# Kernel tuning notes

Hardware: AMD Instinct MI355X
Metric: run time of the kernel (lower is better)

The kernel has to match this reference:

```python
import jax, jax.numpy as jnp
import numpy as np
from jax.scipy.special import logsumexp

NUM_TAGS = 64
BATCH = 512
SEQ = 1024


def setup_inputs() -> dict:
    key = jax.random.key(0)
    k1, k2, k3, k4, k5 = jax.random.split(key, 5)
    emissions = jax.random.normal(k1, (BATCH, SEQ, NUM_TAGS), dtype=jnp.float32)
    # parameters: uniform(-0.1, 0.1) as in reset_parameters
    start_transitions = jax.random.uniform(k2, (NUM_TAGS,), minval=-0.1, maxval=0.1, dtype=jnp.float32)
    end_transitions = jax.random.uniform(k3, (NUM_TAGS,), minval=-0.1, maxval=0.1, dtype=jnp.float32)
    transitions = jax.random.uniform(k4, (NUM_TAGS, NUM_TAGS), minval=-0.1, maxval=0.1, dtype=jnp.float32)
    tags = jax.random.randint(k5, (BATCH, SEQ), 0, NUM_TAGS, dtype=jnp.int64)
    mask = jnp.ones((BATCH, SEQ), dtype=bool)
    return {"emissions": emissions, "start_transitions": start_transitions,
            "end_transitions": end_transitions, "transitions": transitions,
            "tags": tags, "mask": mask}


def _crf_loss(emissions, start_transitions, end_transitions, transitions, tags, mask):
    # batch_first=True -> move to time-major (S, B, T)
    emissions = jnp.transpose(emissions, (1, 0, 2))
    tags = tags.T
    mask = mask.T
    S, B, T = emissions.shape
    maskf = mask.astype(emissions.dtype)

    # ---- joint (numerator) score, fully vectorized ----
    em_sc = jnp.take_along_axis(emissions, tags[:, :, None], axis=2)[:, :, 0]  # [S, B]
    trans_sc = transitions[tags[:-1], tags[1:]]                                # [S-1, B]
    score = start_transitions[tags[0]] + em_sc[0]
    score = score + ((trans_sc + em_sc[1:]) * maskf[1:]).sum(axis=0)
    seq_ends = mask.astype(jnp.int32).sum(axis=0) - 1                          # [B]
    last_tags = tags[seq_ends, jnp.arange(B)]
    score = score + end_transitions[last_tags]

    # ---- log partition (denominator) via scan over time ----
    def step(alphas, xs):
        em_i, m_i = xs  # em_i: [B, T], m_i: [B]
        inner = alphas[:, :, None] + transitions[None, :, :] + em_i[:, None, :]  # [B, T, T]
        new_alphas = logsumexp(inner, axis=1)
        return jnp.where(m_i[:, None], new_alphas, alphas), None

    alphas0 = start_transitions + emissions[0]  # [B, T]
    alphas, _ = jax.lax.scan(step, alphas0, (emissions[1:], mask[1:]))
    log_z = logsumexp(alphas + end_transitions, axis=1)  # [B]

    return (log_z - score).sum()  # reduction='sum'


def reference(emissions, start_transitions, end_transitions, transitions, tags, mask):
    return _crf_loss(emissions, start_transitions, end_transitions, transitions, tags, mask)
```

## Files before the change

kernel.cpp:

```cpp
#include <hip/hip_runtime.h>

#define NT 64
#define SEQ 1024
#define BATCH 512

typedef _Float16 h2 __attribute__((ext_vector_type(2)));
typedef _Float16 h8 __attribute__((ext_vector_type(8)));

__device__ __forceinline__ float rlf(float v, int lane) {
  return __int_as_float(__builtin_amdgcn_readlane(__float_as_int(v), lane));
}
__device__ __forceinline__ float bsum(float v) {
  #pragma unroll
  for (int m = 32; m; m >>= 1) v += __shfl_xor(v, m);
  return v;
}
__device__ __forceinline__ float dot2(h2 a, h2 b, float c) {
#if __has_builtin(__builtin_amdgcn_fdot2)
  return __builtin_amdgcn_fdot2(a, b, c, false);
#else
  return fmaf((float)a[0], (float)b[0], fmaf((float)a[1], (float)b[1], c));
#endif
}

__global__ __launch_bounds__(64) void crf_fwd(
    const float* __restrict__ em,
    const float* __restrict__ startT,
    const float* __restrict__ endT,
    const float* __restrict__ trans,
    const int*   __restrict__ tags,
    float* __restrict__ ws)
{
  const int b = blockIdx.x;
  const int j = threadIdx.x;

  __shared__ float sT[NT * NT];
  __shared__ alignas(16) _Float16 sH[NT];
  for (int i = j; i < NT * NT; i += NT) sT[i] = trans[i];
  __syncthreads();

  h2 eth[NT / 2];
  #pragma unroll
  for (int p = 0; p < NT / 2; ++p) {
    eth[p][0] = (_Float16)(__expf(sT[(2 * p + 0) * NT + j]) * 0.015625f);
    eth[p][1] = (_Float16)(__expf(sT[(2 * p + 1) * NT + j]) * 0.015625f);
  }

  const float* emb = em + (size_t)b * SEQ * NT;
  const int*   tgb = tags + (size_t)b * SEQ;

  const float stv = startT[j];
  const float alpha0 = stv + emb[j];
  const float c0 = rlf(alpha0, 0);
  float nb = __expf(alpha0 - c0);
  sH[j] = (_Float16)nb;

  float Crn = 0.0f;
  float rr = 1.0f;
  float lgrr = 0.0f;

  int tagv = tgb[j];
  const int tag0 = __builtin_amdgcn_readlane(tagv, 0);
  const float sc0 = rlf(stv, tag0);

  float scp = 0.0f;
  {
    int ptag = __shfl_up(tagv, 1);
    if (j > 0) scp += sT[ptag * NT + tagv];
    scp += emb[j * NT + tagv];
  }
  int carry = __builtin_amdgcn_readlane(tagv, 63);

  float embuf[8];
  #pragma unroll
  for (int k = 1; k <= 8; ++k) embuf[k & 7] = emb[k * NT + j];

  auto step = [&](int s, int slot) {
    const float em_cur = embuf[slot];
    int spre = s + 8;
    if (spre > SEQ - 1) spre = SEQ - 1;
    embuf[slot] = emb[spre * NT + j];

    const float mm = __expf(em_cur - 0.5f) * rr;
    Crn -= lgrr;

    float a[8];
    #pragma unroll
    for (int q = 0; q < 8; ++q) {
      const h8 wv = *reinterpret_cast<const h8*>(&sH[8 * q]);
      const h2 w0 = __builtin_shufflevector(wv, wv, 0, 1);
      const h2 w1 = __builtin_shufflevector(wv, wv, 2, 3);
      const h2 w2 = __builtin_shufflevector(wv, wv, 4, 5);
      const h2 w3 = __builtin_shufflevector(wv, wv, 6, 7);
      float acc = dot2(w0, eth[4 * q + 0], 0.0f);
      acc = dot2(w1, eth[4 * q + 1], acc);
      acc = dot2(w2, eth[4 * q + 2], acc);
      acc = dot2(w3, eth[4 * q + 3], acc);
      a[q] = acc;
    }
    const float s01 = (a[0] + a[1]) + (a[2] + a[3]);
    const float s23 = (a[4] + a[5]) + (a[6] + a[7]);
    nb = (s01 + s23) * mm;
    sH[j] = (_Float16)nb;

    const float rv = rlf(nb, 0);
    rr = __builtin_amdgcn_rcpf(rv);
    lgrr = __logf(rr);
  };

  #pragma unroll 8
  for (int r = 1; r < NT; ++r) step(r, r & 7);

  for (int tb = 1; tb < SEQ / NT; ++tb) {
    tagv = tgb[tb * NT + j];
    int ptag = __shfl_up(tagv, 1);
    if (j == 0) ptag = carry;
    scp += sT[ptag * NT + tagv];
    const int base = tb * NT;
    scp += emb[(base + j) * NT + tagv];
    carry = __builtin_amdgcn_readlane(tagv, 63);

    #pragma unroll 8
    for (int r = 0; r < NT; ++r) step(base + r, r & 7);
  }

  const float endv = endT[j];
  const float x = nb * __expf(endv);
  const float tot = bsum(x);
  const float Cbase = c0 + (float)(SEQ - 1) * (0.5f + 4.1588830833596715f);
  const float logz = Cbase + Crn + __logf(tot);

  const float sctot = bsum(scp);
  const float score = sc0 + sctot + rlf(endv, carry);

  if (j == 0) ws[b] = logz - score;
}

__global__ __launch_bounds__(64) void reduce_loss(const float* __restrict__ ws,
                                                  float* __restrict__ out) {
  const int t = threadIdx.x;
  float v = 0.f;
  #pragma unroll
  for (int k = 0; k < BATCH / 64; ++k) v += ws[k * 64 + t];
  const float tot = bsum(v);
  if (t == 0) out[0] = tot;
}

extern "C" void kernel_launch(void* const* d_in, const int* in_sizes, int n_in,
                              void* d_out, int out_size, void* d_ws, size_t ws_size,
                              hipStream_t stream) {
  const float* em    = (const float*)d_in[0];
  const float* st    = (const float*)d_in[1];
  const float* en    = (const float*)d_in[2];
  const float* tr    = (const float*)d_in[3];
  const int*   tags  = (const int*)d_in[4];

  float* ws  = (float*)d_ws;
  float* out = (float*)d_out;

  crf_fwd<<<BATCH, 64, 0, stream>>>(em, st, en, tr, tags, ws);
  reduce_loss<<<1, 64, 0, stream>>>(ws, out);
}
```

Measured before the change: 363.8 us.

## Replace LDS broadcast matvec with cross-lane butterfly reduction and max renormalization

Drops the shared-memory alpha vector and computes the per-step 64x64 transition matvec in registers. Each lane dot-multiplies its own pair of alphas against an XOR-permuted exp-transition table, then a DPP/ds_swizzle/bpermute butterfly tree reduces the partial sums across lanes. Normalization now uses a wave-wide max in place of lane 0's value, which is more robust numerically but adds a serial chain of six cross-lane ops per step. This removes the LDS write and read and their latency on the recurrence's critical path, in exchange for about 31 extra cross-lane permutes per step.

```diff
diff --git a/kernel.cpp b/kernel.cpp
--- a/kernel.cpp
+++ b/kernel.cpp
@@ -5,7 +5,6 @@
 #define BATCH 512
 
 typedef _Float16 h2 __attribute__((ext_vector_type(2)));
-typedef _Float16 h8 __attribute__((ext_vector_type(8)));
 
 __device__ __forceinline__ float rlf(float v, int lane) {
   return __int_as_float(__builtin_amdgcn_readlane(__float_as_int(v), lane));
@@ -14,6 +13,23 @@
   #pragma unroll
   for (int m = 32; m; m >>= 1) v += __shfl_xor(v, m);
   return v;
+}
+__device__ __forceinline__ float bmax(float v) {
+  #pragma unroll
+  for (int m = 32; m; m >>= 1) v = fmaxf(v, __shfl_xor(v, m));
+  return v;
+}
+template <int IMM>
+__device__ __forceinline__ float swzf(float x) {
+  return __int_as_float(__builtin_amdgcn_ds_swizzle(__float_as_int(x), IMM));
+}
+template <int CTRL>
+__device__ __forceinline__ float dppf(float x) {
+  return __int_as_float(
+      __builtin_amdgcn_update_dpp(0, __float_as_int(x), CTRL, 0xF, 0xF, true));
+}
+__device__ __forceinline__ float bpf(int addr, float x) {
+  return __int_as_float(__builtin_amdgcn_ds_bpermute(addr, __float_as_int(x)));
 }
 __device__ __forceinline__ float dot2(h2 a, h2 b, float c) {
 #if __has_builtin(__builtin_amdgcn_fdot2)
@@ -35,15 +51,17 @@
   const int j = threadIdx.x;
 
   __shared__ float sT[NT * NT];
-  __shared__ alignas(16) _Float16 sH[NT];
   for (int i = j; i < NT * NT; i += NT) sT[i] = trans[i];
   __syncthreads();
 
-  h2 eth[NT / 2];
+  const int bp32 = ((j ^ 32) << 2);
+
+  h2 etx[32];
   #pragma unroll
-  for (int p = 0; p < NT / 2; ++p) {
-    eth[p][0] = (_Float16)(__expf(sT[(2 * p + 0) * NT + j]) * 0.015625f);
-    eth[p][1] = (_Float16)(__expf(sT[(2 * p + 1) * NT + j]) * 0.015625f);
+  for (int r = 0; r < 32; ++r) {
+    const int col = j ^ (2 * r);
+    etx[r][0] = (_Float16)(__expf(sT[j * NT + col]) * 0.015625f);
+    etx[r][1] = (_Float16)(__expf(sT[(j ^ 1) * NT + col]) * 0.015625f);
   }
 
   const float* emb = em + (size_t)b * SEQ * NT;
@@ -51,9 +69,8 @@
 
   const float stv = startT[j];
   const float alpha0 = stv + emb[j];
-  const float c0 = rlf(alpha0, 0);
+  const float c0 = bmax(alpha0);
   float nb = __expf(alpha0 - c0);
-  sH[j] = (_Float16)nb;
 
   float Crn = 0.0f;
   float rr = 1.0f;
@@ -84,27 +101,33 @@
     const float mm = __expf(em_cur - 0.5f) * rr;
     Crn -= lgrr;
 
-    float a[8];
+    const float nbx = dppf<0xB1>(nb);
+    const h2 w2 = __builtin_bit_cast(h2, __builtin_amdgcn_cvt_pkrtz(nb, nbx));
+
+    float A[32];
     #pragma unroll
-    for (int q = 0; q < 8; ++q) {
-      const h8 wv = *reinterpret_cast<const h8*>(&sH[8 * q]);
-      const h2 w0 = __builtin_shufflevector(wv, wv, 0, 1);
-      const h2 w1 = __builtin_shufflevector(wv, wv, 2, 3);
-      const h2 w2 = __builtin_shufflevector(wv, wv, 4, 5);
-      const h2 w3 = __builtin_shufflevector(wv, wv, 6, 7);
-      float acc = dot2(w0, eth[4 * q + 0], 0.0f);
-      acc = dot2(w1, eth[4 * q + 1], acc);
-      acc = dot2(w2, eth[4 * q + 2], acc);
-      acc = dot2(w3, eth[4 * q + 3], acc);
-      a[q] = acc;
-    }
-    const float s01 = (a[0] + a[1]) + (a[2] + a[3]);
-    const float s23 = (a[4] + a[5]) + (a[6] + a[7]);
-    nb = (s01 + s23) * mm;
-    sH[j] = (_Float16)nb;
+    for (int r = 0; r < 32; ++r) A[r] = dot2(w2, etx[r], 0.0f);
 
-    const float rv = rlf(nb, 0);
-    rr = __builtin_amdgcn_rcpf(rv);
+    #pragma unroll
+    for (int r = 0; r < 32; r += 2)  A[r] += dppf<0x4E>(A[r | 1]);
+    #pragma unroll
+    for (int r = 0; r < 32; r += 4)  A[r] += swzf<0x101F>(A[r | 2]);
+    #pragma unroll
+    for (int r = 0; r < 32; r += 8)  A[r] += swzf<0x201F>(A[r | 4]);
+    #pragma unroll
+    for (int r = 0; r < 32; r += 16) A[r] += swzf<0x401F>(A[r | 8]);
+    A[0] += bpf(bp32, A[16]);
+
+    nb = A[0] * mm;
+
+    float mx = nb;
+    mx = fmaxf(mx, swzf<0x041F>(mx));
+    mx = fmaxf(mx, swzf<0x081F>(mx));
+    mx = fmaxf(mx, swzf<0x101F>(mx));
+    mx = fmaxf(mx, swzf<0x201F>(mx));
+    mx = fmaxf(mx, swzf<0x401F>(mx));
+    mx = fmaxf(mx, bpf(bp32, mx));
+    rr = __builtin_amdgcn_rcpf(mx);
     lgrr = __logf(rr);
   };
 
@@ -125,8 +148,7 @@
   }
 
   const float endv = endT[j];
-  const float x = nb * __expf(endv);
-  const float tot = bsum(x);
+  const float tot = bsum(nb * __expf(endv));
   const float Cbase = c0 + (float)(SEQ - 1) * (0.5f + 4.1588830833596715f);
   const float logz = Cbase + Crn + __logf(tot);
 
```

New measurement: 703.7 us. 93.4% more time.

## Replace LDS broadcast of alphas with DPP/bpermute cross-lane matvec

Applied to the files above, without the earlier changes.

Each step no longer writes the scaled alpha vector to shared memory and reads it back as 8 packed loads per lane. Each lane now packs its own value with neighbours obtained through DPP swizzles and computes 16 partial dot products against a transition table whose register layout is permuted by an XOR pattern. The partials are routed to their owning lanes with 15 ds_bpermute operations, summed in a tree, and the unroll factor is reduced to 4. The aim is to shorten the per-step serial dependency through LDS, at the cost of more cross-lane permute traffic per step.

```diff
diff --git a/kernel.cpp b/kernel.cpp
--- a/kernel.cpp
+++ b/kernel.cpp
@@ -5,7 +5,6 @@
 #define BATCH 512
 
 typedef _Float16 h2 __attribute__((ext_vector_type(2)));
-typedef _Float16 h8 __attribute__((ext_vector_type(8)));
 
 __device__ __forceinline__ float rlf(float v, int lane) {
   return __int_as_float(__builtin_amdgcn_readlane(__float_as_int(v), lane));
@@ -15,6 +14,13 @@
   for (int m = 32; m; m >>= 1) v += __shfl_xor(v, m);
   return v;
 }
+template <int CTRL>
+__device__ __forceinline__ int dppi(int x) {
+  return __builtin_amdgcn_update_dpp(0, x, CTRL, 0xF, 0xF, true);
+}
+__device__ __forceinline__ float bpf(int addr, float x) {
+  return __int_as_float(__builtin_amdgcn_ds_bpermute(addr, __float_as_int(x)));
+}
 __device__ __forceinline__ float dot2(h2 a, h2 b, float c) {
 #if __has_builtin(__builtin_amdgcn_fdot2)
   return __builtin_amdgcn_fdot2(a, b, c, false);
@@ -23,7 +29,7 @@
 #endif
 }
 
-__global__ __launch_bounds__(64) void crf_fwd(
+__global__ __launch_bounds__(64, 1) void crf_fwd(
     const float* __restrict__ em,
     const float* __restrict__ startT,
     const float* __restrict__ endT,
@@ -35,16 +41,22 @@
   const int j = threadIdx.x;
 
   __shared__ float sT[NT * NT];
-  __shared__ alignas(16) _Float16 sH[NT];
   for (int i = j; i < NT * NT; i += NT) sT[i] = trans[i];
   __syncthreads();
 
-  h2 eth[NT / 2];
+  h2 etxa[16], etxb[16];
   #pragma unroll
-  for (int p = 0; p < NT / 2; ++p) {
-    eth[p][0] = (_Float16)(__expf(sT[(2 * p + 0) * NT + j]) * 0.015625f);
-    eth[p][1] = (_Float16)(__expf(sT[(2 * p + 1) * NT + j]) * 0.015625f);
+  for (int q = 0; q < 16; ++q) {
+    const int c = j ^ (4 * q);
+    etxa[q][0] = (_Float16)(__expf(sT[(j ^ 0) * NT + c]) * 0.015625f);
+    etxa[q][1] = (_Float16)(__expf(sT[(j ^ 1) * NT + c]) * 0.015625f);
+    etxb[q][0] = (_Float16)(__expf(sT[(j ^ 2) * NT + c]) * 0.015625f);
+    etxb[q][1] = (_Float16)(__expf(sT[(j ^ 3) * NT + c]) * 0.015625f);
   }
+
+  int bpa[16];
+  #pragma unroll
+  for (int q = 0; q < 16; ++q) bpa[q] = (j ^ (4 * q)) << 2;
 
   const float* emb = em + (size_t)b * SEQ * NT;
   const int*   tgb = tags + (size_t)b * SEQ;
@@ -53,7 +65,6 @@
   const float alpha0 = stv + emb[j];
   const float c0 = rlf(alpha0, 0);
   float nb = __expf(alpha0 - c0);
-  sH[j] = (_Float16)nb;
 
   float Crn = 0.0f;
   float rr = 1.0f;
@@ -84,31 +95,33 @@
     const float mm = __expf(em_cur - 0.5f) * rr;
     Crn -= lgrr;
 
-    float a[8];
+    const float nbx = __int_as_float(dppi<0xB1>(__float_as_int(nb)));
+    const h2 w01 = __builtin_bit_cast(h2, __builtin_amdgcn_cvt_pkrtz(nb, nbx));
+    const h2 w23 = __builtin_bit_cast(h2, dppi<0x4E>(__builtin_bit_cast(int, w01)));
+
+    float A[16];
     #pragma unroll
-    for (int q = 0; q < 8; ++q) {
-      const h8 wv = *reinterpret_cast<const h8*>(&sH[8 * q]);
-      const h2 w0 = __builtin_shufflevector(wv, wv, 0, 1);
-      const h2 w1 = __builtin_shufflevector(wv, wv, 2, 3);
-      const h2 w2 = __builtin_shufflevector(wv, wv, 4, 5);
-      const h2 w3 = __builtin_shufflevector(wv, wv, 6, 7);
-      float acc = dot2(w0, eth[4 * q + 0], 0.0f);
-      acc = dot2(w1, eth[4 * q + 1], acc);
-      acc = dot2(w2, eth[4 * q + 2], acc);
-      acc = dot2(w3, eth[4 * q + 3], acc);
-      a[q] = acc;
-    }
-    const float s01 = (a[0] + a[1]) + (a[2] + a[3]);
-    const float s23 = (a[4] + a[5]) + (a[6] + a[7]);
-    nb = (s01 + s23) * mm;
-    sH[j] = (_Float16)nb;
+    for (int q = 0; q < 16; ++q)
+      A[q] = dot2(w23, etxb[q], dot2(w01, etxa[q], 0.0f));
+
+    float t[16];
+    t[0] = A[0];
+    #pragma unroll
+    for (int q = 1; q < 16; ++q) t[q] = bpf(bpa[q], A[q]);
+
+    #pragma unroll
+    for (int st = 8; st >= 1; st >>= 1)
+      #pragma unroll
+      for (int q = 0; q < st; ++q) t[q] += t[q + st];
+
+    nb = t[0] * mm;
 
     const float rv = rlf(nb, 0);
     rr = __builtin_amdgcn_rcpf(rv);
     lgrr = __logf(rr);
   };
 
-  #pragma unroll 8
+  #pragma unroll 4
   for (int r = 1; r < NT; ++r) step(r, r & 7);
 
   for (int tb = 1; tb < SEQ / NT; ++tb) {
@@ -120,13 +133,12 @@
     scp += emb[(base + j) * NT + tagv];
     carry = __builtin_amdgcn_readlane(tagv, 63);
 
-    #pragma unroll 8
+    #pragma unroll 4
     for (int r = 0; r < NT; ++r) step(base + r, r & 7);
   }
 
   const float endv = endT[j];
-  const float x = nb * __expf(endv);
-  const float tot = bsum(x);
+  const float tot = bsum(nb * __expf(endv));
   const float Cbase = c0 + (float)(SEQ - 1) * (0.5f + 4.1588830833596715f);
   const float logz = Cbase + Crn + __logf(tot);
 
```

After: 607.4 us. 1.67x slower.
